# Performance work log

Hardware: AMD Instinct MI355X
Metric: run time of the kernel (lower is better)

The kernel has to match this reference:

```python
import jax, jax.numpy as jnp
import numpy as np

TEMPERATURE = 8.0  # sqrt(head_dim=64)

def setup_inputs() -> dict:
    key = jax.random.key(0)
    kq, kk, kv, km, kb = jax.random.split(key, 5)
    B, H, S, D = 2, 16, 2048, 64
    q = jax.random.normal(kq, (B, H, S, D), dtype=jnp.float32)
    k = jax.random.normal(kk, (B, H, S, D), dtype=jnp.float32)
    v = jax.random.normal(kv, (B, H, S, D), dtype=jnp.float32)
    mask = jax.random.randint(km, (B, 1, S, S), 0, 2).astype(bool)
    attn_bias = jax.random.normal(kb, (1, H, S, S), dtype=jnp.float32)
    return {"q": q, "k": k, "v": v, "mask": mask, "attn_bias": attn_bias}

def reference(q, k, v, mask, attn_bias):
    # scores: [B,H,Sq,Sk]
    attn = jnp.einsum("bhqd,bhkd->bhqk", q, k) / TEMPERATURE
    attn = attn + attn_bias
    attn = jnp.where(mask, -jnp.inf, attn)  # masked_fill(mask, -inf)
    attn = jax.nn.softmax(attn, axis=-1)
    # dropout in eval mode (deterministic) -> identity
    out = jnp.einsum("bhqk,bhkd->bhqd", attn, v)
    return (out, attn)
```

## Files before the change

### kernel.cpp

```cpp
#include <hip/hip_runtime.h>

#define BATCH 2
#define NH    16
#define SEQ   2048
#define DH    64
#define NW    8
#define KSPAN 256
#define CHUNK 64
#define NCHK  (KSPAN/CHUNK)
#define SUBT  32

typedef __attribute__((ext_vector_type(8))) short          bf16x8;
typedef __attribute__((ext_vector_type(4))) float          f32x4;
typedef __attribute__((ext_vector_type(2))) unsigned int   u32x2;
typedef __attribute__((ext_vector_type(4))) int            i32x4;

__device__ __forceinline__ unsigned short f2bf(float f) {
    union { float f; unsigned int i; } c;
    c.f = f;
    unsigned int x = c.i;
    x += 0x7fffu + ((x >> 16) & 1u);
    return (unsigned short)(x >> 16);
}
__device__ __forceinline__ unsigned int pkt(float lo, float hi) {
    union { float f; unsigned int u; } a, b;
    a.f = lo; b.f = hi;
    return (b.u & 0xFFFF0000u) | (a.u >> 16);
}
__device__ __forceinline__ float bfu2f(unsigned short u) {
    union { unsigned int i; float f; } c;
    c.i = ((unsigned int)u) << 16;
    return c.f;
}

template<bool ISBYTE>
__global__ __launch_bounds__(512, 2)
void sdpa_fused(const float* __restrict__ qp,
                const float* __restrict__ kp,
                const float* __restrict__ vp,
                const void*  __restrict__ mp,
                const float* __restrict__ bp,
                float* __restrict__ outp,
                float* __restrict__ attnp)
{
    __shared__ __align__(16) unsigned short Pbig[16 * 2048];
    __shared__ __align__(16) float Arena[NW][16 * CHUNK];
    __shared__ float Lsum[NW][16];

    const int tid  = threadIdx.x;
    const int w    = tid >> 6;
    const int lane = tid & 63;
    const int l15  = lane & 15;
    const int g    = lane >> 4;

    const unsigned int* mw = (const unsigned int*)mp;
    if ((__any((int)(mw[lane & 31] > 1u)) != 0) != ISBYTE) return;

    const int bid  = blockIdx.x;
    const int orig = (bid & 7) * 512 + (bid >> 3);
    const int h    = orig >> 8;
    const int rem  = orig & 255;
    const int qt   = rem >> 1;
    const int b    = rem & 1;
    const int bh   = b * NH + h;
    const int qbase = qt * 16;
    const int kw   = w * KSPAN;

    const float* kbh = kp + (size_t)bh * SEQ * DH;
    const float* vbh = vp + (size_t)bh * SEQ * DH;
    char* pivot = (char*)&Arena[w][0];
    char* pbig  = (char*)Pbig;

    bf16x8 qf0, qf1;
    {
        const float* qb = qp + ((size_t)bh * SEQ + qbase + l15) * DH + g * 8;
        #pragma unroll
        for (int j = 0; j < 8; ++j) {
            qf0[j] = (short)f2bf(qb[j]      * 0.125f);
            qf1[j] = (short)f2bf(qb[32 + j] * 0.125f);
        }
    }

    struct KS { f32x4 k[2][4]; };
    auto load_k = [&](int tk, KS& R) {
        const int kb = kw + tk * SUBT;
        #pragma unroll
        for (int mb = 0; mb < 2; ++mb) {
            const float* arow = kbh + (size_t)(kb + 16 * mb + l15) * DH + g * 8;
            R.k[mb][0] = *(const f32x4*)(arow);
            R.k[mb][1] = *(const f32x4*)(arow + 4);
            R.k[mb][2] = *(const f32x4*)(arow + 32);
            R.k[mb][3] = *(const f32x4*)(arow + 36);
        }
    };

    auto produce = [&](const KS& R, int s2) {
        #pragma unroll
        for (int mb = 0; mb < 2; ++mb) {
            union { bf16x8 v; unsigned int u[4]; } A0, A1;
            A0.u[0] = pkt(R.k[mb][0][0], R.k[mb][0][1]);
            A0.u[1] = pkt(R.k[mb][0][2], R.k[mb][0][3]);
            A0.u[2] = pkt(R.k[mb][1][0], R.k[mb][1][1]);
            A0.u[3] = pkt(R.k[mb][1][2], R.k[mb][1][3]);
            A1.u[0] = pkt(R.k[mb][2][0], R.k[mb][2][1]);
            A1.u[1] = pkt(R.k[mb][2][2], R.k[mb][2][3]);
            A1.u[2] = pkt(R.k[mb][3][0], R.k[mb][3][1]);
            A1.u[3] = pkt(R.k[mb][3][2], R.k[mb][3][3]);
            f32x4 c = (f32x4){0.f, 0.f, 0.f, 0.f};
            __builtin_amdgcn_s_setprio(1);
            c = __builtin_amdgcn_mfma_f32_16x16x32_bf16(A0.v, qf0, c, 0, 0, 0);
            c = __builtin_amdgcn_mfma_f32_16x16x32_bf16(A1.v, qf1, c, 0, 0, 0);
            __builtin_amdgcn_s_setprio(0);
            const int byo = (128 * s2 + 64 * mb + 16 * g) ^ ((l15 & 7) << 4);
            *(f32x4*)(pivot + l15 * 256 + byo) = c;
        }
    };

    auto load_bias = [&](int c, f32x4* B) {
        #pragma unroll
        for (int i = 0; i < 4; ++i)
            B[i] = *(const f32x4*)(bp + ((size_t)h * SEQ + qbase + 4 * i + g) * SEQ
                                   + kw + c * CHUNK + 4 * l15);
    };

    float rs[4] = {0.f, 0.f, 0.f, 0.f};

    auto consume = [&](int c, const f32x4* B) {
        #pragma unroll
        for (int i = 0; i < 4; ++i) {
            const int qr = 4 * i + g;
            int m4[4];
            if constexpr (ISBYTE) {
                unsigned int mk = *(const unsigned int*)((const unsigned char*)mp +
                    ((size_t)b * SEQ + qbase + qr) * SEQ + kw + c * CHUNK + 4 * l15);
                #pragma unroll
                for (int j = 0; j < 4; ++j) m4[j] = (int)((mk >> (8 * j)) & 0xFFu);
            } else {
                i32x4 mk = *(const i32x4*)((const int*)mp +
                    ((size_t)b * SEQ + qbase + qr) * SEQ + kw + c * CHUNK + 4 * l15);
                #pragma unroll
                for (int j = 0; j < 4; ++j) m4[j] = mk[j];
            }
            f32x4 p = *(const f32x4*)(pivot + qr * 256 + ((16 * l15) ^ ((qr & 7) << 4)));
            f32x4 pa;
            #pragma unroll
            for (int j = 0; j < 4; ++j)
                pa[j] = m4[j] ? 0.0f : __expf(p[j] + B[i][j]);
            rs[i] += pa[0] + pa[1] + pa[2] + pa[3];
            u32x2 pw;
            pw[0] = pkt(pa[0], pa[1]);
            pw[1] = pkt(pa[2], pa[3]);
            const int byo = (2 * kw + 128 * c + 8 * l15) ^ ((qr & 7) << 4);
            *(u32x2*)(pbig + qr * 4096 + byo) = pw;
        }
    };

    f32x4 accO[4];
    #pragma unroll
    for (int i = 0; i < 4; ++i) accO[i] = (f32x4){0.f, 0.f, 0.f, 0.f};

    auto pv = [&](int c) {
        #pragma unroll
        for (int ks2 = 0; ks2 < 2; ++ks2) {
            const int colg = kw + (2 * c + ks2) * SUBT;
            const int byo = (2 * colg + 16 * g) ^ ((l15 & 7) << 4);
            bf16x8 pf = *(const bf16x8*)(pbig + l15 * 4096 + byo);
            const float* vb2 = vbh + (size_t)colg * DH + 512 * g + l15;
            union { bf16x8 v; unsigned int u[4]; } vf[4];
            #pragma unroll
            for (int nb = 0; nb < 4; ++nb)
                #pragma unroll
                for (int i2 = 0; i2 < 4; ++i2)
                    vf[nb].u[i2] = pkt(vb2[(2 * i2) * 64 + 16 * nb],
                                       vb2[(2 * i2 + 1) * 64 + 16 * nb]);
            __builtin_amdgcn_s_setprio(1);
            #pragma unroll
            for (int nb = 0; nb < 4; ++nb)
                accO[nb] = __builtin_amdgcn_mfma_f32_16x16x32_bf16(pf, vf[nb].v, accO[nb], 0, 0, 0);
            __builtin_amdgcn_s_setprio(0);
        }
    };

    {
        KS RA, RB;
        f32x4 BA[4], BB[4];
        load_k(0, RA);
        load_k(1, RB);
        load_bias(0, BA);

        #pragma unroll
        for (int c = 0; c < NCHK; ++c) {
            f32x4* Bcur = (c & 1) ? BB : BA;
            f32x4* Bnxt = (c & 1) ? BA : BB;
            if (c < NCHK - 1) load_bias(c + 1, Bnxt);
            produce(RA, 0);  load_k((2 * c + 2) & 7, RA);
            produce(RB, 1);  load_k((2 * c + 3) & 7, RB);
            consume(c, Bcur);
            pv(c);
        }
    }

    #pragma unroll
    for (int i = 0; i < 4; ++i) {
        float t = rs[i];
        t += __shfl_xor(t, 1, 64);
        t += __shfl_xor(t, 2, 64);
        t += __shfl_xor(t, 4, 64);
        t += __shfl_xor(t, 8, 64);
        if (l15 == 0) Lsum[w][4 * i + g] = t;
    }
    #pragma unroll
    for (int rr = 0; rr < 4; ++rr)
        #pragma unroll
        for (int nb = 0; nb < 4; ++nb)
            Arena[w][(4 * g + rr) * 64 + 16 * nb + l15] = accO[nb][rr];

    __syncthreads();

    float rv[4];
    #pragma unroll
    for (int i = 0; i < 4; ++i) {
        float s = 0.f;
        #pragma unroll
        for (int ww = 0; ww < NW; ++ww) s += Lsum[ww][4 * i + g];
        rv[i] = 1.0f / s;
    }

    #pragma unroll
    for (int i = 0; i < 4; ++i) {
        const int qr = 4 * i + g;
        #pragma unroll
        for (int u = 0; u < 2; ++u) {
            const int byo = (2 * kw + 256 * u + 16 * l15) ^ ((qr & 7) << 4);
            bf16x8 pb8 = *(const bf16x8*)(pbig + qr * 4096 + byo);
            f32x4 o0, o1;
            #pragma unroll
            for (int j = 0; j < 4; ++j) {
                o0[j] = bfu2f((unsigned short)pb8[j])     * rv[i];
                o1[j] = bfu2f((unsigned short)pb8[4 + j]) * rv[i];
            }
            float* ap = attnp + ((size_t)bh * SEQ + qbase + qr) * SEQ
                        + kw + u * 128 + 8 * l15;
            *(f32x4*)ap       = o0;
            *(f32x4*)(ap + 4) = o1;
        }
    }

    if (w == 0) {
        const int d = lane;
        #pragma unroll
        for (int r = 0; r < 16; ++r) {
            float s = 0.f, o = 0.f;
            #pragma unroll
            for (int ww = 0; ww < NW; ++ww) {
                s += Lsum[ww][r];
                o += Arena[ww][r * 64 + d];
            }
            outp[((size_t)bh * SEQ + qbase + r) * DH + d] = o / s;
        }
    }
}

extern "C" void kernel_launch(void* const* d_in, const int* in_sizes, int n_in,
                              void* d_out, int out_size, void* d_ws, size_t ws_size,
                              hipStream_t stream) {
    const float* qp = (const float*)d_in[0];
    const float* kp = (const float*)d_in[1];
    const float* vp = (const float*)d_in[2];
    const void*  mp = d_in[3];
    const float* bp = (const float*)d_in[4];

    float* outp  = (float*)d_out;
    float* attnp = outp + (size_t)BATCH * NH * SEQ * DH;

    dim3 grid(BATCH * NH * (SEQ / 16)), block(512);
    sdpa_fused<true ><<<grid, block, 0, stream>>>(qp, kp, vp, mp, bp, outp, attnp);
    sdpa_fused<false><<<grid, block, 0, stream>>>(qp, kp, vp, mp, bp, outp, attnp);
}
```

Measured before the change: 551.3 us.

## Pre-convert K to bf16 and V to transposed bf16 in workspace before attention

Adds two prepass kernels: one converts K to bf16, the other converts V to bf16 and transposes it through shared memory, both writing into the workspace buffer. The fused attention kernel then loads bf16 K fragments directly and reads transposed V with vector loads, prefetched ahead of the P·V MFMAs. This replaces the per-block fp32 loads, packing work and strided scalar V gathers that every query tile repeated. The cost is two extra launches and an extra read/write pass over K and V, and the fast path only runs when the workspace is large enough.

```diff
diff --git a/kernel.cpp b/kernel.cpp
--- a/kernel.cpp
+++ b/kernel.cpp
@@ -9,10 +9,12 @@
 #define CHUNK 64
 #define NCHK  (KSPAN/CHUNK)
 #define SUBT  32
+#define KVELEMS ((size_t)BATCH * NH * SEQ * DH)
 
 typedef __attribute__((ext_vector_type(8))) short          bf16x8;
 typedef __attribute__((ext_vector_type(4))) float          f32x4;
 typedef __attribute__((ext_vector_type(2))) unsigned int   u32x2;
+typedef __attribute__((ext_vector_type(4))) unsigned short u16x4;
 typedef __attribute__((ext_vector_type(4))) int            i32x4;
 
 __device__ __forceinline__ unsigned short f2bf(float f) {
@@ -33,13 +35,55 @@
     return c.f;
 }
 
-template<bool ISBYTE>
+__global__ __launch_bounds__(256)
+void cvt_k(const float* __restrict__ src, unsigned short* __restrict__ dst)
+{
+    const size_t total = KVELEMS / 4;
+    for (size_t i = (size_t)blockIdx.x * 256 + threadIdx.x; i < total;
+         i += (size_t)gridDim.x * 256) {
+        f32x4 v = ((const f32x4*)src)[i];
+        u16x4 o;
+        #pragma unroll
+        for (int j = 0; j < 4; ++j) o[j] = f2bf(v[j]);
+        ((u16x4*)dst)[i] = o;
+    }
+}
+
+__global__ __launch_bounds__(256)
+void cvt_vt(const float* __restrict__ vp, unsigned short* __restrict__ vt)
+{
+    __shared__ unsigned short T[64][72];
+    const int bh = blockIdx.x >> 5, kt = blockIdx.x & 31;
+    const int t  = threadIdx.x;
+    const int r  = t >> 2, c0 = (t & 3) * 16;
+    const float* src = vp + ((size_t)bh * SEQ + kt * 64 + r) * DH + c0;
+    #pragma unroll
+    for (int j = 0; j < 4; ++j) {
+        f32x4 v = *(const f32x4*)(src + 4 * j);
+        #pragma unroll
+        for (int jj = 0; jj < 4; ++jj) T[r][c0 + 4 * j + jj] = f2bf(v[jj]);
+    }
+    __syncthreads();
+    const int d = t >> 2, k0 = (t & 3) * 16;
+    unsigned short* dst = vt + ((size_t)bh * DH + d) * SEQ + kt * 64 + k0;
+    #pragma unroll
+    for (int j = 0; j < 4; ++j) {
+        u16x4 o;
+        #pragma unroll
+        for (int jj = 0; jj < 4; ++jj) o[jj] = T[k0 + 4 * j + jj][d];
+        *(u16x4*)(dst + 4 * j) = o;
+    }
+}
+
+template<bool ISBYTE, bool PRE>
 __global__ __launch_bounds__(512, 2)
 void sdpa_fused(const float* __restrict__ qp,
                 const float* __restrict__ kp,
                 const float* __restrict__ vp,
                 const void*  __restrict__ mp,
                 const float* __restrict__ bp,
+                const unsigned short* __restrict__ kb16,
+                const unsigned short* __restrict__ vt16,
                 float* __restrict__ outp,
                 float* __restrict__ attnp)
 {
@@ -68,6 +112,8 @@
 
     const float* kbh = kp + (size_t)bh * SEQ * DH;
     const float* vbh = vp + (size_t)bh * SEQ * DH;
+    const unsigned short* kbh16 = kb16 + (size_t)bh * SEQ * DH;
+    const unsigned short* vth16 = vt16 + ((size_t)bh * DH + l15) * SEQ;
     char* pivot = (char*)&Arena[w][0];
     char* pbig  = (char*)Pbig;
 
@@ -81,35 +127,48 @@
         }
     }
 
-    struct KS { f32x4 k[2][4]; };
+    struct KS { f32x4 kf[2][4]; bf16x8 kh[2][2]; };
     auto load_k = [&](int tk, KS& R) {
         const int kb = kw + tk * SUBT;
         #pragma unroll
         for (int mb = 0; mb < 2; ++mb) {
-            const float* arow = kbh + (size_t)(kb + 16 * mb + l15) * DH + g * 8;
-            R.k[mb][0] = *(const f32x4*)(arow);
-            R.k[mb][1] = *(const f32x4*)(arow + 4);
-            R.k[mb][2] = *(const f32x4*)(arow + 32);
-            R.k[mb][3] = *(const f32x4*)(arow + 36);
+            if constexpr (PRE) {
+                const unsigned short* arow = kbh16 + (size_t)(kb + 16 * mb + l15) * DH + g * 8;
+                R.kh[mb][0] = *(const bf16x8*)(arow);
+                R.kh[mb][1] = *(const bf16x8*)(arow + 32);
+            } else {
+                const float* arow = kbh + (size_t)(kb + 16 * mb + l15) * DH + g * 8;
+                R.kf[mb][0] = *(const f32x4*)(arow);
+                R.kf[mb][1] = *(const f32x4*)(arow + 4);
+                R.kf[mb][2] = *(const f32x4*)(arow + 32);
+                R.kf[mb][3] = *(const f32x4*)(arow + 36);
+            }
         }
     };
 
     auto produce = [&](const KS& R, int s2) {
         #pragma unroll
         for (int mb = 0; mb < 2; ++mb) {
-            union { bf16x8 v; unsigned int u[4]; } A0, A1;
-            A0.u[0] = pkt(R.k[mb][0][0], R.k[mb][0][1]);
-            A0.u[1] = pkt(R.k[mb][0][2], R.k[mb][0][3]);
-            A0.u[2] = pkt(R.k[mb][1][0], R.k[mb][1][1]);
-            A0.u[3] = pkt(R.k[mb][1][2], R.k[mb][1][3]);
-            A1.u[0] = pkt(R.k[mb][2][0], R.k[mb][2][1]);
-            A1.u[1] = pkt(R.k[mb][2][2], R.k[mb][2][3]);
-            A1.u[2] = pkt(R.k[mb][3][0], R.k[mb][3][1]);
-            A1.u[3] = pkt(R.k[mb][3][2], R.k[mb][3][3]);
+            bf16x8 A0, A1;
+            if constexpr (PRE) {
+                A0 = R.kh[mb][0];
+                A1 = R.kh[mb][1];
+            } else {
+                union { bf16x8 v; unsigned int u[4]; } B0, B1;
+                B0.u[0] = pkt(R.kf[mb][0][0], R.kf[mb][0][1]);
+                B0.u[1] = pkt(R.kf[mb][0][2], R.kf[mb][0][3]);
+                B0.u[2] = pkt(R.kf[mb][1][0], R.kf[mb][1][1]);
+                B0.u[3] = pkt(R.kf[mb][1][2], R.kf[mb][1][3]);
+                B1.u[0] = pkt(R.kf[mb][2][0], R.kf[mb][2][1]);
+                B1.u[1] = pkt(R.kf[mb][2][2], R.kf[mb][2][3]);
+                B1.u[2] = pkt(R.kf[mb][3][0], R.kf[mb][3][1]);
+                B1.u[3] = pkt(R.kf[mb][3][2], R.kf[mb][3][3]);
+                A0 = B0.v; A1 = B1.v;
+            }
             f32x4 c = (f32x4){0.f, 0.f, 0.f, 0.f};
             __builtin_amdgcn_s_setprio(1);
-            c = __builtin_amdgcn_mfma_f32_16x16x32_bf16(A0.v, qf0, c, 0, 0, 0);
-            c = __builtin_amdgcn_mfma_f32_16x16x32_bf16(A1.v, qf1, c, 0, 0, 0);
+            c = __builtin_amdgcn_mfma_f32_16x16x32_bf16(A0, qf0, c, 0, 0, 0);
+            c = __builtin_amdgcn_mfma_f32_16x16x32_bf16(A1, qf1, c, 0, 0, 0);
             __builtin_amdgcn_s_setprio(0);
             const int byo = (128 * s2 + 64 * mb + 16 * g) ^ ((l15 & 7) << 4);
             *(f32x4*)(pivot + l15 * 256 + byo) = c;
@@ -159,7 +218,22 @@
     #pragma unroll
     for (int i = 0; i < 4; ++i) accO[i] = (f32x4){0.f, 0.f, 0.f, 0.f};
 
-    auto pv = [&](int c) {
+    auto load_vt = [&](int colg, bf16x8* F) {
+        #pragma unroll
+        for (int nb = 0; nb < 4; ++nb)
+            F[nb] = *(const bf16x8*)(vth16 + (size_t)(16 * nb) * SEQ + colg + 8 * g);
+    };
+    auto pv_pre = [&](int colg, const bf16x8* F) {
+        const int byo = (2 * colg + 16 * g) ^ ((l15 & 7) << 4);
+        bf16x8 pf = *(const bf16x8*)(pbig + l15 * 4096 + byo);
+        __builtin_amdgcn_s_setprio(1);
+        #pragma unroll
+        for (int nb = 0; nb < 4; ++nb)
+            accO[nb] = __builtin_amdgcn_mfma_f32_16x16x32_bf16(pf, F[nb], accO[nb], 0, 0, 0);
+        __builtin_amdgcn_s_setprio(0);
+    };
+
+    auto pv_f32 = [&](int c) {
         #pragma unroll
         for (int ks2 = 0; ks2 < 2; ++ks2) {
             const int colg = kw + (2 * c + ks2) * SUBT;
@@ -184,6 +258,7 @@
     {
         KS RA, RB;
         f32x4 BA[4], BB[4];
+        bf16x8 V0[4], V1[4];
         load_k(0, RA);
         load_k(1, RB);
         load_bias(0, BA);
@@ -192,11 +267,18 @@
         for (int c = 0; c < NCHK; ++c) {
             f32x4* Bcur = (c & 1) ? BB : BA;
             f32x4* Bnxt = (c & 1) ? BA : BB;
+            if constexpr (PRE) load_vt(kw + (2 * c) * SUBT, V0);
             if (c < NCHK - 1) load_bias(c + 1, Bnxt);
             produce(RA, 0);  load_k((2 * c + 2) & 7, RA);
             produce(RB, 1);  load_k((2 * c + 3) & 7, RB);
+            if constexpr (PRE) load_vt(kw + (2 * c + 1) * SUBT, V1);
             consume(c, Bcur);
-            pv(c);
+            if constexpr (PRE) {
+                pv_pre(kw + (2 * c) * SUBT, V0);
+                pv_pre(kw + (2 * c + 1) * SUBT, V1);
+            } else {
+                pv_f32(c);
+            }
         }
     }
 
@@ -273,7 +355,19 @@
     float* outp  = (float*)d_out;
     float* attnp = outp + (size_t)BATCH * NH * SEQ * DH;
 
+    unsigned short* kb16 = (unsigned short*)d_ws;
+    unsigned short* vt16 = kb16 + KVELEMS;
+    const bool usePre = ws_size >= 2 * KVELEMS * sizeof(unsigned short);
+
     dim3 grid(BATCH * NH * (SEQ / 16)), block(512);
-    sdpa_fused<true ><<<grid, block, 0, stream>>>(qp, kp, vp, mp, bp, outp, attnp);
-    sdpa_fused<false><<<grid, block, 0, stream>>>(qp, kp, vp, mp, bp, outp, attnp);
-}
+
+    if (usePre) {
+        cvt_k <<<dim3(1024), dim3(256), 0, stream>>>(kp, kb16);
+        cvt_vt<<<dim3(BATCH * NH * 32), dim3(256), 0, stream>>>(vp, vt16);
+        sdpa_fused<true , true ><<<grid, block, 0, stream>>>(qp, kp, vp, mp, bp, kb16, vt16, outp, attnp);
+        sdpa_fused<false, true ><<<grid, block, 0, stream>>>(qp, kp, vp, mp, bp, kb16, vt16, outp, attnp);
+    } else {
+        sdpa_fused<true , false><<<grid, block, 0, stream>>>(qp, kp, vp, mp, bp, kb16, vt16, outp, attnp);
+        sdpa_fused<false, false><<<grid, block, 0, stream>>>(qp, kp, vp, mp, bp, kb16, vt16, outp, attnp);
+    }
+}
```

Measured after the change: 490.3 us. 11.1% less time.
